# Optimization experiments

Hardware: AMD Instinct MI355X
Metric: run time of the kernel (lower is better)

The kernel has to match this reference:

```python
import jax, jax.numpy as jnp
import numpy as np

B, T, F = 32, 4096, 512
H = 512

def setup_inputs() -> dict:
    key = jax.random.key(0)
    k1, k2, k3, k4, k5 = jax.random.split(key, 5)
    enc = jax.random.normal(k1, (B, T, F), dtype=jnp.float32)
    dec = jax.random.normal(k2, (B, F), dtype=jnp.float32)
    # Dense kernels (no bias), scaled like Glorot-ish init
    W1 = jax.random.normal(k3, (F, H), dtype=jnp.float32) / np.sqrt(F)
    W2 = jax.random.normal(k4, (F, H), dtype=jnp.float32) / np.sqrt(F)
    V = jax.random.normal(k5, (H, 1), dtype=jnp.float32) / np.sqrt(H)
    return {"encoder_outputs": enc, "dec_output": dec, "W1": W1, "W2": W2, "V": V}

def reference(encoder_outputs, dec_output, W1, W2, V):
    # Bahdanau additive attention, fully vectorized over time_steps
    # (the original runs this step-by-step via K.rnn; state is unchanged,
    # so the computation is embarrassingly parallel over t).
    w1_e = jnp.einsum('btf,fh->bth', encoder_outputs, W1)   # [B,T,H]
    w2_d = jnp.einsum('bf,fh->bh', dec_output, W2)          # [B,H]
    scores = jnp.einsum('bth,h->bt', jnp.tanh(w1_e + w2_d[:, None, :]), V[:, 0])  # [B,T]
    return jax.nn.softmax(scores, axis=1)
```

## Files before the change

kernel.cpp:

```cpp
#include <hip/hip_runtime.h>
#include <hip/hip_bf16.h>

#define B_ 32
#define T_ 4096
#define F_ 512
#define H_ 512

typedef float floatx4 __attribute__((ext_vector_type(4)));
typedef short short8 __attribute__((ext_vector_type(8)));

__device__ __forceinline__ unsigned short f2bf16(float a) {
  unsigned ua = __float_as_uint(a);
  return (unsigned short)((ua + 0x7FFFu + ((ua >> 16) & 1u)) >> 16);
}

__device__ __forceinline__ float tanh_fast(float x) {
  float e = __expf(2.0f * x);
  return 1.0f - __fdividef(2.0f, e + 1.0f);
}

__device__ __forceinline__ short8 cvt8(float4 lo, float4 hi) {
  union { short8 s8; __hip_bfloat16 h[8]; } u;
  u.h[0] = __float2bfloat16(lo.x);
  u.h[1] = __float2bfloat16(lo.y);
  u.h[2] = __float2bfloat16(lo.z);
  u.h[3] = __float2bfloat16(lo.w);
  u.h[4] = __float2bfloat16(hi.x);
  u.h[5] = __float2bfloat16(hi.y);
  u.h[6] = __float2bfloat16(hi.z);
  u.h[7] = __float2bfloat16(hi.w);
  return u.s8;
}

__global__ __launch_bounds__(1024) void prep_all(const float* __restrict__ W1,
                                                 unsigned short* __restrict__ W1T,
                                                 const float* __restrict__ dec,
                                                 const float* __restrict__ W2,
                                                 float* __restrict__ w2d,
                                                 float* __restrict__ scores) {
  __shared__ float tile[32][33];
  if (blockIdx.x < 256) {
    const int tx = threadIdx.x & 31, ty = threadIdx.x >> 5;
    const int bx = blockIdx.x & 15, by = blockIdx.x >> 4;
    const int f = by * 32 + ty;
    const int h = bx * 32 + tx;
    tile[ty][tx] = W1[f * H_ + h];
    __syncthreads();
    const int ho = bx * 32 + ty;
    const int fo = by * 32 + tx;
    W1T[ho * F_ + fo] = f2bf16(tile[tx][ty]);
  } else if (blockIdx.x < 272) {
    const int g = (blockIdx.x - 256) * 1024 + threadIdx.x;
    const int b = g >> 9;
    const int h = g & 511;
    float s0 = 0.f, s1 = 0.f, s2 = 0.f, s3 = 0.f;
    for (int f = 0; f < F_; f += 4) {
      s0 += dec[b * F_ + f + 0] * W2[(f + 0) * H_ + h];
      s1 += dec[b * F_ + f + 1] * W2[(f + 1) * H_ + h];
      s2 += dec[b * F_ + f + 2] * W2[(f + 2) * H_ + h];
      s3 += dec[b * F_ + f + 3] * W2[(f + 3) * H_ + h];
    }
    w2d[b * H_ + h] = (s0 + s1) + (s2 + s3);
  } else {
    const int g = (blockIdx.x - 272) * 1024 + threadIdx.x;
    const float4 z = {0.f, 0.f, 0.f, 0.f};
    ((float4*)scores)[g * 2 + 0] = z;
    ((float4*)scores)[g * 2 + 1] = z;
  }
}

__global__ __launch_bounds__(256, 3) void fused_score(
    const float* __restrict__ enc, const unsigned short* __restrict__ W1T,
    const float* __restrict__ w2d, const float* __restrict__ V,
    float* __restrict__ scores) {
  __shared__ __align__(16) unsigned short As[2][128 * 40];
  __shared__ __align__(16) unsigned short Bs[3][128 * 32];

  const int tid = threadIdx.x;
  const int bid = blockIdx.x;
  const int xcd = bid & 7;
  const int ii = bid >> 3;
  const int n_blk = ii & 3;
  const int m_blk = xcd + ((ii >> 2) << 3);
  const int lane = tid & 63;
  const int wave = tid >> 6;
  const int wm = wave >> 1;
  const int wn = wave & 1;
  const int quad = lane >> 4;
  const int l16 = lane & 15;

  const int arow = tid >> 2;
  const int acol = (tid & 3) * 8;
  const float* aptr = enc + (size_t)(m_blk * 128 + arow) * F_ + acol;

  const int nb0 = wave * 32;
  const int bl_n = lane >> 2;
  const int bl_c = (lane & 3) ^ ((lane >> 3) & 3);
  const unsigned short* bsrc0 =
      W1T + (size_t)(n_blk * 128 + nb0 + bl_n) * F_ + bl_c * 8;
  const unsigned short* bsrc1 = bsrc0 + 16 * F_;

  floatx4 acc[4][4];
#pragma unroll
  for (int i = 0; i < 4; i++)
#pragma unroll
    for (int j = 0; j < 4; j++) acc[i][j] = (floatx4){0.f, 0.f, 0.f, 0.f};

  float4 a_pre[4];

#define GLDS(SRC, DST)                                                       \
  __builtin_amdgcn_global_load_lds(                                          \
      (const __attribute__((address_space(1))) void*)(SRC),                  \
      (__attribute__((address_space(3))) void*)(DST), 16, 0, 0)

#pragma unroll
  for (int rr = 0; rr < 2; ++rr) {
    a_pre[rr * 2 + 0] = *(const float4*)(aptr + rr * 64 * F_ + 0);
    a_pre[rr * 2 + 1] = *(const float4*)(aptr + rr * 64 * F_ + 4);
  }
  GLDS(bsrc0, &Bs[0][nb0 * 32]);
  GLDS(bsrc1, &Bs[0][(nb0 + 16) * 32]);
  GLDS(bsrc0 + 32, &Bs[1][nb0 * 32]);
  GLDS(bsrc1 + 32, &Bs[1][(nb0 + 16) * 32]);
#pragma unroll
  for (int rr = 0; rr < 2; ++rr) {
    short8 pk = cvt8(a_pre[rr * 2 + 0], a_pre[rr * 2 + 1]);
    *(short8*)&As[0][(arow + rr * 64) * 40 + acol] = pk;
  }
  asm volatile("s_waitcnt vmcnt(2) lgkmcnt(0)" ::: "memory");
  __builtin_amdgcn_s_barrier();

#pragma unroll
  for (int ks = 0; ks < 16; ++ks) {
    const int cur3 = ks % 3;
    const int cur2 = ks & 1;

    if (ks < 15) {
      const int k1 = (ks + 1) * 32;
#pragma unroll
      for (int rr = 0; rr < 2; ++rr) {
        a_pre[rr * 2 + 0] = *(const float4*)(aptr + rr * 64 * F_ + k1);
        a_pre[rr * 2 + 1] = *(const float4*)(aptr + rr * 64 * F_ + k1 + 4);
      }
    }
    if (ks < 14) {
      const int nb3 = (ks + 2) % 3;
      const int k2 = (ks + 2) * 32;
      GLDS(bsrc0 + k2, &Bs[nb3][nb0 * 32]);
      GLDS(bsrc1 + k2, &Bs[nb3][(nb0 + 16) * 32]);
    }

    short8 af[4], bfr[4];
#pragma unroll
    for (int i = 0; i < 4; i++)
      af[i] = *(const short8*)&As[cur2][(wm * 64 + i * 16 + l16) * 40 + quad * 8];
#pragma unroll
    for (int j = 0; j < 4; j++)
      bfr[j] = *(const short8*)&Bs[cur3][(wn * 64 + j * 16 + l16) * 32 +
                                         ((quad ^ ((l16 >> 1) & 3)) * 8)];
#pragma unroll
    for (int i = 0; i < 4; i++)
#pragma unroll
      for (int j = 0; j < 4; j++)
        acc[i][j] = __builtin_amdgcn_mfma_f32_16x16x32_bf16(af[i], bfr[j], acc[i][j], 0, 0, 0);

    if (ks < 15) {
#pragma unroll
      for (int rr = 0; rr < 2; ++rr) {
        short8 pk = cvt8(a_pre[rr * 2 + 0], a_pre[rr * 2 + 1]);
        *(short8*)&As[cur2 ^ 1][(arow + rr * 64) * 40 + acol] = pk;
      }
    }

    if (ks < 14) {
      asm volatile("s_waitcnt vmcnt(2) lgkmcnt(0)" ::: "memory");
      __builtin_amdgcn_s_barrier();
    } else if (ks == 14) {
      asm volatile("s_waitcnt vmcnt(0) lgkmcnt(0)" ::: "memory");
      __builtin_amdgcn_s_barrier();
    }
  }
#undef GLDS

  const int b = m_blk >> 5;
  float w2v[4], vv[4];
#pragma unroll
  for (int j = 0; j < 4; j++) {
    const int h = n_blk * 128 + wn * 64 + j * 16 + l16;
    w2v[j] = w2d[b * H_ + h];
    vv[j] = V[h];
  }
  float rs[4][4];
#pragma unroll
  for (int i = 0; i < 4; i++)
#pragma unroll
    for (int r = 0; r < 4; r++) {
      float s = 0.f;
#pragma unroll
      for (int j = 0; j < 4; j++) s += tanh_fast(acc[i][j][r] + w2v[j]) * vv[j];
      rs[i][r] = s;
    }
#pragma unroll
  for (int i = 0; i < 4; i++)
#pragma unroll
    for (int r = 0; r < 4; r++) {
      float s = rs[i][r];
      s += __shfl_xor(s, 1, 16);
      s += __shfl_xor(s, 2, 16);
      s += __shfl_xor(s, 4, 16);
      s += __shfl_xor(s, 8, 16);
      rs[i][r] = s;
    }
  if (l16 == 0) {
#pragma unroll
    for (int i = 0; i < 4; i++)
#pragma unroll
      for (int r = 0; r < 4; r++)
        atomicAdd(&scores[m_blk * 128 + wm * 64 + i * 16 + quad * 4 + r], rs[i][r]);
  }
}

__global__ __launch_bounds__(256) void softmax_rows(const float* __restrict__ scores,
                                                    float* __restrict__ out) {
  const int b = blockIdx.x;
  const int tid = threadIdx.x;
  const int wave = tid >> 6;
  __shared__ float red[4];
  float v[16];
  float mx = -1e30f;
#pragma unroll
  for (int i = 0; i < 16; i++) {
    v[i] = scores[b * T_ + i * 256 + tid];
    mx = fmaxf(mx, v[i]);
  }
#pragma unroll
  for (int o = 32; o > 0; o >>= 1) mx = fmaxf(mx, __shfl_xor(mx, o, 64));
  if ((tid & 63) == 0) red[wave] = mx;
  __syncthreads();
  mx = fmaxf(fmaxf(red[0], red[1]), fmaxf(red[2], red[3]));
  __syncthreads();
  float sum = 0.f;
#pragma unroll
  for (int i = 0; i < 16; i++) {
    v[i] = __expf(v[i] - mx);
    sum += v[i];
  }
#pragma unroll
  for (int o = 32; o > 0; o >>= 1) sum += __shfl_xor(sum, o, 64);
  if ((tid & 63) == 0) red[wave] = sum;
  __syncthreads();
  sum = (red[0] + red[1]) + (red[2] + red[3]);
  const float inv = 1.0f / sum;
#pragma unroll
  for (int i = 0; i < 16; i++) out[b * T_ + i * 256 + tid] = v[i] * inv;
}

extern "C" void kernel_launch(void* const* d_in, const int* in_sizes, int n_in,
                              void* d_out, int out_size, void* d_ws, size_t ws_size,
                              hipStream_t stream) {
  const float* enc = (const float*)d_in[0];
  const float* dec = (const float*)d_in[1];
  const float* W1 = (const float*)d_in[2];
  const float* W2 = (const float*)d_in[3];
  const float* V = (const float*)d_in[4];
  float* out = (float*)d_out;

  char* ws = (char*)d_ws;
  float* scores = (float*)ws;
  unsigned short* W1T = (unsigned short*)(ws + 524288);
  float* w2d = (float*)(ws + 1048576);

  (void)in_sizes; (void)n_in; (void)out_size; (void)ws_size;

  prep_all<<<dim3(288), dim3(1024), 0, stream>>>(W1, W1T, dec, W2, w2d, scores);
  fused_score<<<dim3(4096), dim3(256), 0, stream>>>(enc, W1T, w2d, V, scores);
  softmax_rows<<<dim3(32), dim3(256), 0, stream>>>(scores, out);
}
```

Baseline: 513.3 us.

## Prefetch A tiles two steps ahead, swizzle A LDS, raise occupancy

Encoder (A) loads now run two k-steps ahead using a double set of prefetch registers, matching the depth of the B pipeline, so global latency gets more time to hide. The padded A shared-memory layout (stride 40) becomes an unpadded stride-32 layout with an XOR swizzle, which cuts LDS use. Launch bounds go from 3 to 4 blocks per CU. The extra prefetch registers together with the tighter occupancy target could cause register pressure or spills.

```diff
diff --git a/kernel.cpp b/kernel.cpp
--- a/kernel.cpp
+++ b/kernel.cpp
@@ -69,11 +69,11 @@
   }
 }
 
-__global__ __launch_bounds__(256, 3) void fused_score(
+__global__ __launch_bounds__(256, 4) void fused_score(
     const float* __restrict__ enc, const unsigned short* __restrict__ W1T,
     const float* __restrict__ w2d, const float* __restrict__ V,
     float* __restrict__ scores) {
-  __shared__ __align__(16) unsigned short As[2][128 * 40];
+  __shared__ __align__(16) unsigned short As[2][128 * 32];
   __shared__ __align__(16) unsigned short Bs[3][128 * 32];
 
   const int tid = threadIdx.x;
@@ -90,8 +90,9 @@
   const int l16 = lane & 15;
 
   const int arow = tid >> 2;
-  const int acol = (tid & 3) * 8;
-  const float* aptr = enc + (size_t)(m_blk * 128 + arow) * F_ + acol;
+  const int achk = tid & 3;
+  const float* aptr = enc + (size_t)(m_blk * 128 + arow) * F_ + achk * 8;
+  const int aslot = (achk ^ ((arow >> 1) & 3)) * 8;
 
   const int nb0 = wave * 32;
   const int bl_n = lane >> 2;
@@ -106,74 +107,71 @@
 #pragma unroll
     for (int j = 0; j < 4; j++) acc[i][j] = (floatx4){0.f, 0.f, 0.f, 0.f};
 
-  float4 a_pre[4];
+  float4 a_pre[2][4];
 
 #define GLDS(SRC, DST)                                                       \
   __builtin_amdgcn_global_load_lds(                                          \
       (const __attribute__((address_space(1))) void*)(SRC),                  \
       (__attribute__((address_space(3))) void*)(DST), 16, 0, 0)
 
-#pragma unroll
-  for (int rr = 0; rr < 2; ++rr) {
-    a_pre[rr * 2 + 0] = *(const float4*)(aptr + rr * 64 * F_ + 0);
-    a_pre[rr * 2 + 1] = *(const float4*)(aptr + rr * 64 * F_ + 4);
-  }
-  GLDS(bsrc0, &Bs[0][nb0 * 32]);
-  GLDS(bsrc1, &Bs[0][(nb0 + 16) * 32]);
-  GLDS(bsrc0 + 32, &Bs[1][nb0 * 32]);
-  GLDS(bsrc1 + 32, &Bs[1][(nb0 + 16) * 32]);
-#pragma unroll
-  for (int rr = 0; rr < 2; ++rr) {
-    short8 pk = cvt8(a_pre[rr * 2 + 0], a_pre[rr * 2 + 1]);
-    *(short8*)&As[0][(arow + rr * 64) * 40 + acol] = pk;
-  }
-  asm volatile("s_waitcnt vmcnt(2) lgkmcnt(0)" ::: "memory");
+#define A_ISSUE(PAR, K)                                                      \
+  do {                                                                       \
+    a_pre[PAR][0] = *(const float4*)(aptr + (K));                            \
+    a_pre[PAR][1] = *(const float4*)(aptr + (K) + 4);                        \
+    a_pre[PAR][2] = *(const float4*)(aptr + 64 * F_ + (K));                  \
+    a_pre[PAR][3] = *(const float4*)(aptr + 64 * F_ + (K) + 4);              \
+  } while (0)
+
+#define A_WRITE(PAR, BUF)                                                    \
+  do {                                                                       \
+    short8 pk0 = cvt8(a_pre[PAR][0], a_pre[PAR][1]);                         \
+    short8 pk1 = cvt8(a_pre[PAR][2], a_pre[PAR][3]);                         \
+    *(short8*)&As[BUF][arow * 32 + aslot] = pk0;                             \
+    *(short8*)&As[BUF][(arow + 64) * 32 + aslot] = pk1;                      \
+  } while (0)
+
+#define B_ISSUE(BUF, K)                                                      \
+  do {                                                                       \
+    GLDS(bsrc0 + (K), &Bs[BUF][nb0 * 32]);                                   \
+    GLDS(bsrc1 + (K), &Bs[BUF][(nb0 + 16) * 32]);                            \
+  } while (0)
+
+  A_ISSUE(0, 0);
+  B_ISSUE(0, 0);
+  B_ISSUE(1, 32);
+  A_ISSUE(1, 32);
+  A_WRITE(0, 0);
+  asm volatile("s_waitcnt vmcnt(6) lgkmcnt(0)" ::: "memory");
   __builtin_amdgcn_s_barrier();
 
 #pragma unroll
   for (int ks = 0; ks < 16; ++ks) {
-    const int cur3 = ks % 3;
-    const int cur2 = ks & 1;
-
-    if (ks < 15) {
-      const int k1 = (ks + 1) * 32;
-#pragma unroll
-      for (int rr = 0; rr < 2; ++rr) {
-        a_pre[rr * 2 + 0] = *(const float4*)(aptr + rr * 64 * F_ + k1);
-        a_pre[rr * 2 + 1] = *(const float4*)(aptr + rr * 64 * F_ + k1 + 4);
-      }
-    }
-    if (ks < 14) {
-      const int nb3 = (ks + 2) % 3;
-      const int k2 = (ks + 2) * 32;
-      GLDS(bsrc0 + k2, &Bs[nb3][nb0 * 32]);
-      GLDS(bsrc1 + k2, &Bs[nb3][(nb0 + 16) * 32]);
+    if (ks <= 13) {
+      A_ISSUE(ks & 1, (ks + 2) * 32);
+      B_ISSUE((ks + 2) % 3, (ks + 2) * 32);
     }
 
     short8 af[4], bfr[4];
 #pragma unroll
     for (int i = 0; i < 4; i++)
-      af[i] = *(const short8*)&As[cur2][(wm * 64 + i * 16 + l16) * 40 + quad * 8];
+      af[i] = *(const short8*)&As[ks & 1][(wm * 64 + i * 16 + l16) * 32 +
+                                          ((quad ^ ((l16 >> 1) & 3)) * 8)];
 #pragma unroll
     for (int j = 0; j < 4; j++)
-      bfr[j] = *(const short8*)&Bs[cur3][(wn * 64 + j * 16 + l16) * 32 +
-                                         ((quad ^ ((l16 >> 1) & 3)) * 8)];
+      bfr[j] = *(const short8*)&Bs[ks % 3][(wn * 64 + j * 16 + l16) * 32 +
+                                           ((quad ^ ((l16 >> 1) & 3)) * 8)];
 #pragma unroll
     for (int i = 0; i < 4; i++)
 #pragma unroll
       for (int j = 0; j < 4; j++)
         acc[i][j] = __builtin_amdgcn_mfma_f32_16x16x32_bf16(af[i], bfr[j], acc[i][j], 0, 0, 0);
 
-    if (ks < 15) {
-#pragma unroll
-      for (int rr = 0; rr < 2; ++rr) {
-        short8 pk = cvt8(a_pre[rr * 2 + 0], a_pre[rr * 2 + 1]);
-        *(short8*)&As[cur2 ^ 1][(arow + rr * 64) * 40 + acol] = pk;
-      }
-    }
-
-    if (ks < 14) {
-      asm volatile("s_waitcnt vmcnt(2) lgkmcnt(0)" ::: "memory");
+    if (ks <= 14) {
+      A_WRITE((ks + 1) & 1, (ks + 1) & 1);
+    }
+
+    if (ks <= 13) {
+      asm volatile("s_waitcnt vmcnt(6) lgkmcnt(0)" ::: "memory");
       __builtin_amdgcn_s_barrier();
     } else if (ks == 14) {
       asm volatile("s_waitcnt vmcnt(0) lgkmcnt(0)" ::: "memory");
@@ -181,6 +179,9 @@
     }
   }
 #undef GLDS
+#undef A_ISSUE
+#undef A_WRITE
+#undef B_ISSUE
 
   const int b = m_blk >> 5;
   float w2v[4], vv[4];
```

Result: faster. 477.6 us (-6.9%).
